# Performance work log

Hardware: AMD Instinct MI355X
Metric: run time of the kernel (lower is better)

The kernel has to match this reference:

```python
import jax, jax.numpy as jnp
import numpy as np

CUTOFF = 3  # cutoff_freq default in low_pass_filter


def _low_pass(x):
    # full 2D FFT over (H, W), keep only the 4 corner blocks of size CUTOFF
    H, W = x.shape[-2], x.shape[-1]
    f = jnp.fft.fftn(x, axes=(-2, -1))
    mask = jnp.zeros((H, W), dtype=x.dtype)
    c = CUTOFF
    mask = mask.at[:c, :c].set(1).at[:c, -c:].set(1).at[-c:, :c].set(1).at[-c:, -c:].set(1)
    return jnp.abs(jnp.fft.ifftn(f * mask, axes=(-2, -1)))


def setup_inputs() -> dict:
    key = jax.random.key(0)
    k_x, k_w1, k_b1, k_w2, k_b2 = jax.random.split(key, 5)
    n_feat = 8
    B, C, H, W = 32, 3, 512, 512
    x = jax.random.uniform(k_x, (B, C, H, W), dtype=jnp.float32)
    # 1x1 convs == channel-mixing matrices; kaiming-ish scale
    w1 = jax.random.normal(k_w1, (n_feat, C), dtype=jnp.float32) * (1.0 / np.sqrt(C))
    b1 = jax.random.normal(k_b1, (n_feat,), dtype=jnp.float32) * 0.01
    w2 = jax.random.normal(k_w2, (C, n_feat), dtype=jnp.float32) * (1.0 / np.sqrt(n_feat))
    b2 = jax.random.normal(k_b2, (C,), dtype=jnp.float32) * 0.01
    return {"x": x, "w1": w1, "b1": b1, "w2": w2, "b2": b2}


def reference(x, w1, b1, w2, b2):
    lp = _low_pass(x)                                        # [B,3,H,W]
    h = jax.nn.relu(jnp.einsum('bchw,fc->bfhw', lp, w1) + b1[None, :, None, None])
    y = jnp.einsum('bfhw,cf->bchw', h, w2) + b2[None, :, None, None]
    return jnp.clip(y + lp, 0.0, 1.0)
```

## Files before the change

### kernel.cpp

```cpp
#include <hip/hip_runtime.h>
#include <math.h>


#define WS_TS 0
#define WS_F  6144
#define WS_A  12288
constexpr int NPART = 8;
constexpr int ROWS = 32;

__global__ __launch_bounds__(256) void k_tab(float* __restrict__ ws) {
    int h = blockIdx.x * 256 + threadIdx.x;
    if (h >= 512) return;
    const float STEP = 6.28318530717958647692f / 512.0f;
    const int mv[6] = {0, 1, 2, -3, -2, -1};
    float* tsp = ws + WS_TS + h * 12;
#pragma unroll
    for (int i = 0; i < 6; ++i) {
        int r = ((mv[i] * h) % 512 + 512) & 511;
        float s, c;
        sincosf(STEP * (float)r, &s, &c);
        tsp[2 * i] = c; tsp[2 * i + 1] = s;
    }
}

__global__ __launch_bounds__(256) void k_colsum(const float* __restrict__ x,
                                                float* __restrict__ ws) {
    __shared__ float Xc[128][29];
    float* A = ws + WS_A;
    int img = blockIdx.x >> 3;
    int hgp = blockIdx.x & 7;
    int t = threadIdx.x;
    int wq = t & 127;
    int hl = t >> 7;
    int h0 = (hgp * 2 + hl) * ROWS;
    const float* xp = x + (size_t)img * 262144 + (size_t)h0 * 512 + wq * 4;

    const float TH = 6.28318530717958647692f / 512.0f;
    float pc1, ps1, pc2, ps2, pc3, ps3;
    sincosf(TH * (float)h0, &ps1, &pc1);
    pc2 = pc1 * pc1 - ps1 * ps1;  ps2 = 2.f * pc1 * ps1;
    pc3 = pc1 * pc2 - ps1 * ps2;  ps3 = ps1 * pc2 + pc1 * ps2;
    const float C1 = 0.99992470183914450299f, S1 = 0.01227153828571992539f;
    const float C2 = 0.99969881869620422012f, S2 = 0.02454122852291228803f;
    const float C3 = 0.99932238458834954375f, S3 = 0.03680722294135883171f;

    float s0[4] = {0,0,0,0};
    float ar1[4] = {0,0,0,0}, ai1[4] = {0,0,0,0};
    float ar2[4] = {0,0,0,0}, ai2[4] = {0,0,0,0};
    float ar3[4] = {0,0,0,0}, ai3[4] = {0,0,0,0};

#pragma unroll 4
    for (int i = 0; i < ROWS; ++i) {
        float4 xv = *(const float4*)(xp + (size_t)i * 512);
        float xa[4] = {xv.x, xv.y, xv.z, xv.w};
#pragma unroll
        for (int q = 0; q < 4; ++q) {
            s0[q] += xa[q];
            ar1[q] = fmaf(xa[q], pc1, ar1[q]);  ai1[q] = fmaf(-xa[q], ps1, ai1[q]);
            ar2[q] = fmaf(xa[q], pc2, ar2[q]);  ai2[q] = fmaf(-xa[q], ps2, ai2[q]);
            ar3[q] = fmaf(xa[q], pc3, ar3[q]);  ai3[q] = fmaf(-xa[q], ps3, ai3[q]);
        }
        float n;
        n = pc1 * C1 - ps1 * S1;  ps1 = ps1 * C1 + pc1 * S1;  pc1 = n;
        n = pc2 * C2 - ps2 * S2;  ps2 = ps2 * C2 + pc2 * S2;  pc2 = n;
        n = pc3 * C3 - ps3 * S3;  ps3 = ps3 * C3 + pc3 * S3;  pc3 = n;
    }

    if (hl == 1) {
        float* r = &Xc[wq][0];
#pragma unroll
        for (int q = 0; q < 4; ++q) {
            r[q]      = s0[q];
            r[4 + q]  = ar1[q];  r[8 + q]  = ai1[q];
            r[12 + q] = ar2[q];  r[16 + q] = ai2[q];
            r[20 + q] = ar3[q];  r[24 + q] = ai3[q];
        }
    }
    __syncthreads();
    if (hl == 0) {
        const float* r = &Xc[wq][0];
        float* Ab = A + (((size_t)img * NPART + hgp) * 8) * 512 + wq * 4;
        *(float4*)(Ab + 0 * 512) = make_float4(s0[0] + r[0], s0[1] + r[1], s0[2] + r[2], s0[3] + r[3]);
        *(float4*)(Ab + 1 * 512) = make_float4(0.f, 0.f, 0.f, 0.f);
        *(float4*)(Ab + 2 * 512) = make_float4(ar1[0] + r[4],  ar1[1] + r[5],  ar1[2] + r[6],  ar1[3] + r[7]);
        *(float4*)(Ab + 3 * 512) = make_float4(ai1[0] + r[8],  ai1[1] + r[9],  ai1[2] + r[10], ai1[3] + r[11]);
        *(float4*)(Ab + 4 * 512) = make_float4(ar2[0] + r[12], ar2[1] + r[13], ar2[2] + r[14], ar2[3] + r[15]);
        *(float4*)(Ab + 5 * 512) = make_float4(ai2[0] + r[16], ai2[1] + r[17], ai2[2] + r[18], ai2[3] + r[19]);
        *(float4*)(Ab + 6 * 512) = make_float4(ar3[0] + r[20], ar3[1] + r[21], ar3[2] + r[22], ar3[3] + r[23]);
        *(float4*)(Ab + 7 * 512) = make_float4(ai3[0] + r[24], ai3[1] + r[25], ai3[2] + r[26], ai3[3] + r[27]);
    }
}

__global__ __launch_bounds__(256) void k_proj(float* __restrict__ ws) {
    __shared__ float As[8][8][68];
    __shared__ float Rs[28][8][2];
    const float* A = ws + WS_A;
    float* F = ws + WS_F;
    int img = blockIdx.x;
    int t = threadIdx.x;

    {
        int plane = t >> 5;
        int w0 = (t & 31) * 16;
        float4 acc[4];
#pragma unroll
        for (int q = 0; q < 4; ++q) acc[q] = make_float4(0.f, 0.f, 0.f, 0.f);
        const float* base = A + ((size_t)img * NPART * 8 + plane) * 512 + w0;
        for (int hg = 0; hg < NPART; ++hg) {
            const float* p = base + (size_t)hg * 8 * 512;
#pragma unroll
            for (int q = 0; q < 4; ++q) {
                float4 v = *(const float4*)(p + q * 4);
                acc[q].x += v.x; acc[q].y += v.y; acc[q].z += v.z; acc[q].w += v.w;
            }
        }
        int seg = w0 >> 6, j0 = w0 & 63;
#pragma unroll
        for (int q = 0; q < 4; ++q)
            *(float4*)&As[plane][seg][j0 + q * 4] = acc[q];
    }
    __syncthreads();

    if (t < 224) {
        int pair = t >> 3, seg = t & 7;
        int k = pair / 7, mi = pair % 7;
        float m = (float)(mi - 3);
        const float TH = 6.28318530717958647692f / 512.0f;
        float cm, sm, pc, ps;
        sincosf(-m * TH, &sm, &cm);
        sincosf(-m * TH * (float)(seg * 64), &ps, &pc);
        const float* Ar_ = &As[2 * k][seg][0];
        const float* Ai_ = &As[2 * k + 1][seg][0];
        float pre = 0.f, pim = 0.f;
#pragma unroll 4
        for (int j = 0; j < 64; ++j) {
            float Ar = Ar_[j], Ai = Ai_[j];
            pre += Ar * pc - Ai * ps;
            pim += Ar * ps + Ai * pc;
            float n = pc * cm - ps * sm;
            ps = ps * cm + pc * sm;
            pc = n;
        }
        Rs[pair][seg][0] = pre;
        Rs[pair][seg][1] = pim;
    }
    __syncthreads();
    if (t < 56) {
        int pair = t >> 1, part = t & 1;
        float s = 0.f;
#pragma unroll
        for (int g = 0; g < 8; ++g) s += Rs[pair][g][part];
        F[(size_t)img * 56 + t] = s;
    }
}

__global__ __launch_bounds__(256) void k_out(const float* __restrict__ ws,
                                             const float* __restrict__ w1,
                                             const float* __restrict__ b1,
                                             const float* __restrict__ w2,
                                             const float* __restrict__ b2,
                                             float* __restrict__ out) {
    const float* tabS = ws + WS_TS;
    const float* Fb = ws + WS_F;
    __shared__ float F_lds[3][56];
    __shared__ float T[4][3][12];
    int t = threadIdx.x;
    int blk = blockIdx.x;
    int b = blk >> 7;
    int h0 = (blk & 127) << 2;

    if (t < 168) {
        int c = t / 56, comp = t % 56;
        F_lds[c][comp] = Fb[(size_t)(b * 3 + c) * 56 + comp];
    }

    float rw1[8][3], rb1[8], rw2[3][8], rb2[3];
#pragma unroll
    for (int f_ = 0; f_ < 8; ++f_) {
        rb1[f_] = b1[f_];
#pragma unroll
        for (int c = 0; c < 3; ++c) rw1[f_][c] = w1[f_ * 3 + c];
    }
#pragma unroll
    for (int c = 0; c < 3; ++c) {
        rb2[c] = b2[c];
#pragma unroll
        for (int f_ = 0; f_ < 8; ++f_) rw2[c][f_] = w2[c * 8 + f_];
    }
    __syncthreads();

    if (t < 72) {
        int rl = t / 18, rem = t % 18;
        int c = rem / 6, kc = rem % 6;
        int h = h0 + rl;
        const float* th = tabS + h * 12;
        int m_kc = (kc < 3) ? kc : kc - 6;
        const float inv = 1.0f / (512.0f * 512.0f);
        float tre = 0.f, tim = 0.f;
#pragma unroll
        for (int kr = 0; kr < 6; ++kr) {
            int kk, mi; float csign;
            if (kr < 3) { kk = kr;     mi = m_kc + 3; csign =  1.f; }
            else        { kk = 6 - kr; mi = 3 - m_kc; csign = -1.f; }
            int pair = kk * 7 + mi;
            float fr = F_lds[c][pair * 2] * inv;
            float fi = F_lds[c][pair * 2 + 1] * csign * inv;
            float cc = th[kr * 2], ss = th[kr * 2 + 1];
            tre += fr * cc - fi * ss;
            tim += fr * ss + fi * cc;
        }
        T[rl][c][kc * 2]     = tre;
        T[rl][c][kc * 2 + 1] = tim;
    }
    __syncthreads();

    int rl = t >> 6, lane = t & 63;
    int h = h0 + rl;
    float A0r[3], A0i[3], U1r[3], U1i[3], V1r[3], V1i[3];
    float U2r[3], U2i[3], V2r[3], V2i[3], Br[3], Bi[3];
#pragma unroll
    for (int c = 0; c < 3; ++c) {
        const float* Tc = T[rl][c];
        A0r[c] = Tc[0];  A0i[c] = Tc[1];
        float t1r = Tc[2],  t1i = Tc[3];
        float t2r = Tc[4],  t2i = Tc[5];
        float bmr = Tc[6],  bmi = Tc[7];
        float m2r = Tc[8],  m2i = Tc[9];
        float m1r = Tc[10], m1i = Tc[11];
        U1r[c] = t1r + m1r; U1i[c] = t1i + m1i;
        V1r[c] = t1r - m1r; V1i[c] = t1i - m1i;
        U2r[c] = t2r + m2r; U2i[c] = t2i + m2i;
        V2r[c] = t2r - m2r; V2i[c] = t2i - m2i;
        Br[c] = bmr; Bi[c] = bmi;
    }
    const float* tw = tabS + lane * 12;
    float c1 = tw[2], s1 = tw[3];
    float c2 = tw[4], s2 = tw[5];
    float c3 = tw[6], s3 = -tw[7];
    const float K = 0.70710678118654752440f;
    float* ob = out + ((size_t)(b * 3) * 512 + h) * 512;

#pragma unroll
    for (int j = 0; j < 8; ++j) {
        int w = lane + 64 * j;
        float lp[3];
#pragma unroll
        for (int c = 0; c < 3; ++c) {
            float re = A0r[c] + U1r[c] * c1 - V1i[c] * s1
                              + U2r[c] * c2 - V2i[c] * s2
                              + Br[c] * c3 + Bi[c] * s3;
            float im = A0i[c] + U1i[c] * c1 + V1r[c] * s1
                              + U2i[c] * c2 + V2r[c] * s2
                              + Bi[c] * c3 - Br[c] * s3;
            lp[c] = sqrtf(re * re + im * im);
        }
        float hid[8];
#pragma unroll
        for (int f_ = 0; f_ < 8; ++f_) {
            float v = rb1[f_] + lp[0] * rw1[f_][0] + lp[1] * rw1[f_][1] + lp[2] * rw1[f_][2];
            hid[f_] = fmaxf(v, 0.0f);
        }
#pragma unroll
        for (int c = 0; c < 3; ++c) {
            float y = rb2[c] + lp[c];
#pragma unroll
            for (int f_ = 0; f_ < 8; ++f_) y += hid[f_] * rw2[c][f_];
            y = fminf(fmaxf(y, 0.0f), 1.0f);
            ob[(size_t)c * 262144 + w] = y;
        }
        if (j < 7) {
            float nc1 = K * (c1 - s1), ns1 = K * (c1 + s1);
            float nc2 = -s2,           ns2 = c2;
            float nc3 = -K * (c3 + s3), ns3 = K * (c3 - s3);
            c1 = nc1; s1 = ns1; c2 = nc2; s2 = ns2; c3 = nc3; s3 = ns3;
        }
    }
}

extern "C" void kernel_launch(void* const* d_in, const int* in_sizes, int n_in,
                              void* d_out, int out_size, void* d_ws, size_t ws_size,
                              hipStream_t stream) {
    const float* x  = (const float*)d_in[0];
    const float* w1 = (const float*)d_in[1];
    const float* b1 = (const float*)d_in[2];
    const float* w2 = (const float*)d_in[3];
    const float* b2 = (const float*)d_in[4];
    float* out = (float*)d_out;
    float* ws = (float*)d_ws;

    hipLaunchKernelGGL(k_tab, dim3(2), dim3(256), 0, stream, ws);
    hipLaunchKernelGGL(k_colsum, dim3(96 * 8), dim3(256), 0, stream, x, ws);
    hipLaunchKernelGGL(k_proj, dim3(96), dim3(256), 0, stream, ws);
    hipLaunchKernelGGL(k_out, dim3(4096), dim3(256), 0, stream, ws, w1, b1, w2, b2, out);
}
```

Baseline: 71.02 us.

## Widen colsum blocks with register prefetch and fold twiddle table into proj

The column-sum kernel now uses 512 threads per block, with four row-groups of 16 rows each instead of two of 32. It prefetches the next four rows into registers while the current four are accumulated, and reduces the partial sums through a larger shared buffer. The twiddle-table kernel is removed and its work moved to an extra block of k_proj, saving one launch. This trades a shorter dependency chain and more memory-level parallelism for extra register pressure and a larger shared reduction.

```diff
diff --git a/kernel.cpp b/kernel.cpp
--- a/kernel.cpp
+++ b/kernel.cpp
@@ -6,33 +6,17 @@
 #define WS_F  6144
 #define WS_A  12288
 constexpr int NPART = 8;
-constexpr int ROWS = 32;
-
-__global__ __launch_bounds__(256) void k_tab(float* __restrict__ ws) {
-    int h = blockIdx.x * 256 + threadIdx.x;
-    if (h >= 512) return;
-    const float STEP = 6.28318530717958647692f / 512.0f;
-    const int mv[6] = {0, 1, 2, -3, -2, -1};
-    float* tsp = ws + WS_TS + h * 12;
-#pragma unroll
-    for (int i = 0; i < 6; ++i) {
-        int r = ((mv[i] * h) % 512 + 512) & 511;
-        float s, c;
-        sincosf(STEP * (float)r, &s, &c);
-        tsp[2 * i] = c; tsp[2 * i + 1] = s;
-    }
-}
-
-__global__ __launch_bounds__(256) void k_colsum(const float* __restrict__ x,
-                                                float* __restrict__ ws) {
-    __shared__ float Xc[128][29];
+
+__global__ __launch_bounds__(512, 6) void k_colsum(const float* __restrict__ x,
+                                                   float* __restrict__ ws) {
+    __shared__ float buf[3][128][29];
     float* A = ws + WS_A;
     int img = blockIdx.x >> 3;
-    int hgp = blockIdx.x & 7;
+    int slab = blockIdx.x & 7;
     int t = threadIdx.x;
     int wq = t & 127;
-    int hl = t >> 7;
-    int h0 = (hgp * 2 + hl) * ROWS;
+    int q = t >> 7;
+    int h0 = slab * 64 + q * 16;
     const float* xp = x + (size_t)img * 262144 + (size_t)h0 * 512 + wq * 4;
 
     const float TH = 6.28318530717958647692f / 512.0f;
@@ -49,75 +33,112 @@
     float ar2[4] = {0,0,0,0}, ai2[4] = {0,0,0,0};
     float ar3[4] = {0,0,0,0}, ai3[4] = {0,0,0,0};
 
-#pragma unroll 4
-    for (int i = 0; i < ROWS; ++i) {
-        float4 xv = *(const float4*)(xp + (size_t)i * 512);
-        float xa[4] = {xv.x, xv.y, xv.z, xv.w};
-#pragma unroll
-        for (int q = 0; q < 4; ++q) {
-            s0[q] += xa[q];
-            ar1[q] = fmaf(xa[q], pc1, ar1[q]);  ai1[q] = fmaf(-xa[q], ps1, ai1[q]);
-            ar2[q] = fmaf(xa[q], pc2, ar2[q]);  ai2[q] = fmaf(-xa[q], ps2, ai2[q]);
-            ar3[q] = fmaf(xa[q], pc3, ar3[q]);  ai3[q] = fmaf(-xa[q], ps3, ai3[q]);
-        }
-        float n;
-        n = pc1 * C1 - ps1 * S1;  ps1 = ps1 * C1 + pc1 * S1;  pc1 = n;
-        n = pc2 * C2 - ps2 * S2;  ps2 = ps2 * C2 + pc2 * S2;  pc2 = n;
-        n = pc3 * C3 - ps3 * S3;  ps3 = ps3 * C3 + pc3 * S3;  pc3 = n;
-    }
-
-    if (hl == 1) {
-        float* r = &Xc[wq][0];
-#pragma unroll
-        for (int q = 0; q < 4; ++q) {
-            r[q]      = s0[q];
-            r[4 + q]  = ar1[q];  r[8 + q]  = ai1[q];
-            r[12 + q] = ar2[q];  r[16 + q] = ai2[q];
-            r[20 + q] = ar3[q];  r[24 + q] = ai3[q];
-        }
-    }
-    __syncthreads();
-    if (hl == 0) {
-        const float* r = &Xc[wq][0];
-        float* Ab = A + (((size_t)img * NPART + hgp) * 8) * 512 + wq * 4;
-        *(float4*)(Ab + 0 * 512) = make_float4(s0[0] + r[0], s0[1] + r[1], s0[2] + r[2], s0[3] + r[3]);
+    float4 cur[4], nxt[4];
+#pragma unroll
+    for (int j = 0; j < 4; ++j) cur[j] = *(const float4*)(xp + (size_t)j * 512);
+#pragma unroll
+    for (int g = 0; g < 4; ++g) {
+        if (g < 3) {
+#pragma unroll
+            for (int j = 0; j < 4; ++j)
+                nxt[j] = *(const float4*)(xp + (size_t)((g + 1) * 4 + j) * 512);
+        }
+#pragma unroll
+        for (int j = 0; j < 4; ++j) {
+            float xa[4] = {cur[j].x, cur[j].y, cur[j].z, cur[j].w};
+#pragma unroll
+            for (int u = 0; u < 4; ++u) {
+                s0[u] += xa[u];
+                ar1[u] = fmaf(xa[u], pc1, ar1[u]);  ai1[u] = fmaf(-xa[u], ps1, ai1[u]);
+                ar2[u] = fmaf(xa[u], pc2, ar2[u]);  ai2[u] = fmaf(-xa[u], ps2, ai2[u]);
+                ar3[u] = fmaf(xa[u], pc3, ar3[u]);  ai3[u] = fmaf(-xa[u], ps3, ai3[u]);
+            }
+            float n;
+            n = pc1 * C1 - ps1 * S1;  ps1 = ps1 * C1 + pc1 * S1;  pc1 = n;
+            n = pc2 * C2 - ps2 * S2;  ps2 = ps2 * C2 + pc2 * S2;  pc2 = n;
+            n = pc3 * C3 - ps3 * S3;  ps3 = ps3 * C3 + pc3 * S3;  pc3 = n;
+        }
+#pragma unroll
+        for (int j = 0; j < 4; ++j) cur[j] = nxt[j];
+    }
+
+    if (q != 0) {
+        float* r = &buf[q - 1][wq][0];
+#pragma unroll
+        for (int u = 0; u < 4; ++u) {
+            r[u]      = s0[u];
+            r[4 + u]  = ar1[u];  r[8 + u]  = ai1[u];
+            r[12 + u] = ar2[u];  r[16 + u] = ai2[u];
+            r[20 + u] = ar3[u];  r[24 + u] = ai3[u];
+        }
+    }
+    __syncthreads();
+    if (q == 0) {
+#pragma unroll
+        for (int v = 0; v < 3; ++v) {
+            const float* r = &buf[v][wq][0];
+#pragma unroll
+            for (int u = 0; u < 4; ++u) {
+                s0[u]  += r[u];
+                ar1[u] += r[4 + u];   ai1[u] += r[8 + u];
+                ar2[u] += r[12 + u];  ai2[u] += r[16 + u];
+                ar3[u] += r[20 + u];  ai3[u] += r[24 + u];
+            }
+        }
+        float* Ab = A + (((size_t)img * NPART + slab) * 8) * 512 + wq * 4;
+        *(float4*)(Ab + 0 * 512) = make_float4(s0[0], s0[1], s0[2], s0[3]);
         *(float4*)(Ab + 1 * 512) = make_float4(0.f, 0.f, 0.f, 0.f);
-        *(float4*)(Ab + 2 * 512) = make_float4(ar1[0] + r[4],  ar1[1] + r[5],  ar1[2] + r[6],  ar1[3] + r[7]);
-        *(float4*)(Ab + 3 * 512) = make_float4(ai1[0] + r[8],  ai1[1] + r[9],  ai1[2] + r[10], ai1[3] + r[11]);
-        *(float4*)(Ab + 4 * 512) = make_float4(ar2[0] + r[12], ar2[1] + r[13], ar2[2] + r[14], ar2[3] + r[15]);
-        *(float4*)(Ab + 5 * 512) = make_float4(ai2[0] + r[16], ai2[1] + r[17], ai2[2] + r[18], ai2[3] + r[19]);
-        *(float4*)(Ab + 6 * 512) = make_float4(ar3[0] + r[20], ar3[1] + r[21], ar3[2] + r[22], ar3[3] + r[23]);
-        *(float4*)(Ab + 7 * 512) = make_float4(ai3[0] + r[24], ai3[1] + r[25], ai3[2] + r[26], ai3[3] + r[27]);
+        *(float4*)(Ab + 2 * 512) = make_float4(ar1[0], ar1[1], ar1[2], ar1[3]);
+        *(float4*)(Ab + 3 * 512) = make_float4(ai1[0], ai1[1], ai1[2], ai1[3]);
+        *(float4*)(Ab + 4 * 512) = make_float4(ar2[0], ar2[1], ar2[2], ar2[3]);
+        *(float4*)(Ab + 5 * 512) = make_float4(ai2[0], ai2[1], ai2[2], ai2[3]);
+        *(float4*)(Ab + 6 * 512) = make_float4(ar3[0], ar3[1], ar3[2], ar3[3]);
+        *(float4*)(Ab + 7 * 512) = make_float4(ai3[0], ai3[1], ai3[2], ai3[3]);
     }
 }
 
 __global__ __launch_bounds__(256) void k_proj(float* __restrict__ ws) {
+    int t = threadIdx.x;
+    if (blockIdx.x == 96) {
+        const float STEP = 6.28318530717958647692f / 512.0f;
+        const int mv[6] = {0, 1, 2, -3, -2, -1};
+        for (int h = t; h < 512; h += 256) {
+            float* tsp = ws + WS_TS + h * 12;
+#pragma unroll
+            for (int i = 0; i < 6; ++i) {
+                int r = ((mv[i] * h) % 512 + 512) & 511;
+                float s, c;
+                sincosf(STEP * (float)r, &s, &c);
+                tsp[2 * i] = c; tsp[2 * i + 1] = s;
+            }
+        }
+        return;
+    }
     __shared__ float As[8][8][68];
     __shared__ float Rs[28][8][2];
     const float* A = ws + WS_A;
     float* F = ws + WS_F;
     int img = blockIdx.x;
-    int t = threadIdx.x;
 
     {
         int plane = t >> 5;
         int w0 = (t & 31) * 16;
         float4 acc[4];
 #pragma unroll
-        for (int q = 0; q < 4; ++q) acc[q] = make_float4(0.f, 0.f, 0.f, 0.f);
+        for (int u = 0; u < 4; ++u) acc[u] = make_float4(0.f, 0.f, 0.f, 0.f);
         const float* base = A + ((size_t)img * NPART * 8 + plane) * 512 + w0;
         for (int hg = 0; hg < NPART; ++hg) {
             const float* p = base + (size_t)hg * 8 * 512;
 #pragma unroll
-            for (int q = 0; q < 4; ++q) {
-                float4 v = *(const float4*)(p + q * 4);
-                acc[q].x += v.x; acc[q].y += v.y; acc[q].z += v.z; acc[q].w += v.w;
+            for (int u = 0; u < 4; ++u) {
+                float4 v = *(const float4*)(p + u * 4);
+                acc[u].x += v.x; acc[u].y += v.y; acc[u].z += v.z; acc[u].w += v.w;
             }
         }
         int seg = w0 >> 6, j0 = w0 & 63;
 #pragma unroll
-        for (int q = 0; q < 4; ++q)
-            *(float4*)&As[plane][seg][j0 + q * 4] = acc[q];
+        for (int u = 0; u < 4; ++u)
+            *(float4*)&As[plane][seg][j0 + u * 4] = acc[u];
     }
     __syncthreads();
 
@@ -288,8 +309,7 @@
     float* out = (float*)d_out;
     float* ws = (float*)d_ws;
 
-    hipLaunchKernelGGL(k_tab, dim3(2), dim3(256), 0, stream, ws);
-    hipLaunchKernelGGL(k_colsum, dim3(96 * 8), dim3(256), 0, stream, x, ws);
-    hipLaunchKernelGGL(k_proj, dim3(96), dim3(256), 0, stream, ws);
+    hipLaunchKernelGGL(k_colsum, dim3(96 * NPART), dim3(512), 0, stream, x, ws);
+    hipLaunchKernelGGL(k_proj, dim3(97), dim3(256), 0, stream, ws);
     hipLaunchKernelGGL(k_out, dim3(4096), dim3(256), 0, stream, ws, w1, b1, w2, b2, out);
 }
```

Result: no change. 69.74 us (-1.8%).

## Restructure column-sum loads, split projection across segments, fold table into proj

Applied to the files above, without the earlier changes.

k_colsum now uses 4 waves per block, each handling 16 rows with two float4 loads per row (two column halves), batched loads of 8 rows, and twiddles recomputed per row from a base angle. Partials from the other waves are reduced through shared memory. k_proj is split into 8 blocks per image, one per 64-column segment, and the final segment sum moves into k_out. The twiddle table kernel is folded into an extra block of k_proj, which removes one launch. These changes aim to raise memory-level parallelism and increase block count on the small stages, at the cost of extra partial-sum traffic and more registers.

```diff
diff --git a/kernel.cpp b/kernel.cpp
--- a/kernel.cpp
+++ b/kernel.cpp
@@ -3,134 +3,162 @@
 
 
 #define WS_TS 0
-#define WS_F  6144
-#define WS_A  12288
+#define WS_PP 8192
+#define WS_A  65536
 constexpr int NPART = 8;
-constexpr int ROWS = 32;
-
-__global__ __launch_bounds__(256) void k_tab(float* __restrict__ ws) {
-    int h = blockIdx.x * 256 + threadIdx.x;
-    if (h >= 512) return;
-    const float STEP = 6.28318530717958647692f / 512.0f;
-    const int mv[6] = {0, 1, 2, -3, -2, -1};
-    float* tsp = ws + WS_TS + h * 12;
-#pragma unroll
-    for (int i = 0; i < 6; ++i) {
-        int r = ((mv[i] * h) % 512 + 512) & 511;
-        float s, c;
-        sincosf(STEP * (float)r, &s, &c);
-        tsp[2 * i] = c; tsp[2 * i + 1] = s;
-    }
-}
-
-__global__ __launch_bounds__(256) void k_colsum(const float* __restrict__ x,
-                                                float* __restrict__ ws) {
-    __shared__ float Xc[128][29];
+
+#define CJ1 0.99992470183914450299f
+#define CJ2 0.99969881869620422012f
+#define CJ3 0.99932238458834954375f
+#define CJ4 0.99879545620517239271f
+#define SJ1 0.01227153828571992539f
+#define SJ2 0.02454122852291228803f
+#define SJ3 0.03680722294135883171f
+#define SJ4 0.04906767432741801425f
+
+__global__ __launch_bounds__(256, 4) void k_colsum(const float* __restrict__ x,
+                                                   float* __restrict__ ws) {
+    __shared__ float buf[3][64][57];
     float* A = ws + WS_A;
     int img = blockIdx.x >> 3;
-    int hgp = blockIdx.x & 7;
+    int hgrp = blockIdx.x & 7;
     int t = threadIdx.x;
-    int wq = t & 127;
-    int hl = t >> 7;
-    int h0 = (hgp * 2 + hl) * ROWS;
-    const float* xp = x + (size_t)img * 262144 + (size_t)h0 * 512 + wq * 4;
+    int v = t >> 6;
+    int lane = t & 63;
+    int R0 = hgrp * 64 + v * 16;
+    const float* xb = x + (size_t)img * 262144 + (size_t)R0 * 512 + lane * 4;
 
     const float TH = 6.28318530717958647692f / 512.0f;
-    float pc1, ps1, pc2, ps2, pc3, ps3;
-    sincosf(TH * (float)h0, &ps1, &pc1);
-    pc2 = pc1 * pc1 - ps1 * ps1;  ps2 = 2.f * pc1 * ps1;
-    pc3 = pc1 * pc2 - ps1 * ps2;  ps3 = ps1 * pc2 + pc1 * ps2;
-    const float C1 = 0.99992470183914450299f, S1 = 0.01227153828571992539f;
-    const float C2 = 0.99969881869620422012f, S2 = 0.02454122852291228803f;
-    const float C3 = 0.99932238458834954375f, S3 = 0.03680722294135883171f;
-
-    float s0[4] = {0,0,0,0};
-    float ar1[4] = {0,0,0,0}, ai1[4] = {0,0,0,0};
-    float ar2[4] = {0,0,0,0}, ai2[4] = {0,0,0,0};
-    float ar3[4] = {0,0,0,0}, ai3[4] = {0,0,0,0};
-
-#pragma unroll 4
-    for (int i = 0; i < ROWS; ++i) {
-        float4 xv = *(const float4*)(xp + (size_t)i * 512);
-        float xa[4] = {xv.x, xv.y, xv.z, xv.w};
-#pragma unroll
-        for (int q = 0; q < 4; ++q) {
-            s0[q] += xa[q];
-            ar1[q] = fmaf(xa[q], pc1, ar1[q]);  ai1[q] = fmaf(-xa[q], ps1, ai1[q]);
-            ar2[q] = fmaf(xa[q], pc2, ar2[q]);  ai2[q] = fmaf(-xa[q], ps2, ai2[q]);
-            ar3[q] = fmaf(xa[q], pc3, ar3[q]);  ai3[q] = fmaf(-xa[q], ps3, ai3[q]);
-        }
-        float n;
-        n = pc1 * C1 - ps1 * S1;  ps1 = ps1 * C1 + pc1 * S1;  pc1 = n;
-        n = pc2 * C2 - ps2 * S2;  ps2 = ps2 * C2 + pc2 * S2;  pc2 = n;
-        n = pc3 * C3 - ps3 * S3;  ps3 = ps3 * C3 + pc3 * S3;  pc3 = n;
-    }
-
-    if (hl == 1) {
-        float* r = &Xc[wq][0];
-#pragma unroll
-        for (int q = 0; q < 4; ++q) {
-            r[q]      = s0[q];
-            r[4 + q]  = ar1[q];  r[8 + q]  = ai1[q];
-            r[12 + q] = ar2[q];  r[16 + q] = ai2[q];
-            r[20 + q] = ar3[q];  r[24 + q] = ai3[q];
-        }
+    float bc, bs;
+    sincosf(TH * (float)R0, &bs, &bc);
+
+    float aA[7][4], aB[7][4];
+#pragma unroll
+    for (int c = 0; c < 7; ++c)
+#pragma unroll
+        for (int q = 0; q < 4; ++q) { aA[c][q] = 0.f; aB[c][q] = 0.f; }
+
+    const float CJr[4] = {1.f, CJ1, CJ2, CJ3};
+    const float SJr[4] = {0.f, SJ1, SJ2, SJ3};
+
+#pragma unroll
+    for (int b = 0; b < 4; ++b) {
+        float4 L[8];
+#pragma unroll
+        for (int rr = 0; rr < 4; ++rr) {
+            L[rr * 2 + 0] = *(const float4*)(xb + (size_t)(b * 4 + rr) * 512);
+            L[rr * 2 + 1] = *(const float4*)(xb + (size_t)(b * 4 + rr) * 512 + 256);
+        }
+#pragma unroll
+        for (int rr = 0; rr < 4; ++rr) {
+            float c1 = bc * CJr[rr] - bs * SJr[rr];
+            float s1 = bs * CJr[rr] + bc * SJr[rr];
+            float c2 = c1 * c1 - s1 * s1;
+            float s2 = 2.f * c1 * s1;
+            float c3 = c1 * c2 - s1 * s2;
+            float s3 = s1 * c2 + c1 * s2;
+            float xa[4] = {L[rr * 2].x, L[rr * 2].y, L[rr * 2].z, L[rr * 2].w};
+            float xbv[4] = {L[rr * 2 + 1].x, L[rr * 2 + 1].y, L[rr * 2 + 1].z, L[rr * 2 + 1].w};
+#pragma unroll
+            for (int q = 0; q < 4; ++q) {
+                aA[0][q] += xa[q];
+                aA[1][q] = fmaf(xa[q], c1, aA[1][q]);  aA[2][q] = fmaf(-xa[q], s1, aA[2][q]);
+                aA[3][q] = fmaf(xa[q], c2, aA[3][q]);  aA[4][q] = fmaf(-xa[q], s2, aA[4][q]);
+                aA[5][q] = fmaf(xa[q], c3, aA[5][q]);  aA[6][q] = fmaf(-xa[q], s3, aA[6][q]);
+                aB[0][q] += xbv[q];
+                aB[1][q] = fmaf(xbv[q], c1, aB[1][q]); aB[2][q] = fmaf(-xbv[q], s1, aB[2][q]);
+                aB[3][q] = fmaf(xbv[q], c2, aB[3][q]); aB[4][q] = fmaf(-xbv[q], s2, aB[4][q]);
+                aB[5][q] = fmaf(xbv[q], c3, aB[5][q]); aB[6][q] = fmaf(-xbv[q], s3, aB[6][q]);
+            }
+        }
+        if (b < 3) {
+            float nb = bc * CJ4 - bs * SJ4;
+            bs = bs * CJ4 + bc * SJ4;
+            bc = nb;
+        }
+    }
+
+    if (v != 0) {
+        float* r = &buf[v - 1][lane][0];
+#pragma unroll
+        for (int c = 0; c < 7; ++c)
+#pragma unroll
+            for (int q = 0; q < 4; ++q) {
+                r[c * 4 + q] = aA[c][q];
+                r[28 + c * 4 + q] = aB[c][q];
+            }
     }
     __syncthreads();
-    if (hl == 0) {
-        const float* r = &Xc[wq][0];
-        float* Ab = A + (((size_t)img * NPART + hgp) * 8) * 512 + wq * 4;
-        *(float4*)(Ab + 0 * 512) = make_float4(s0[0] + r[0], s0[1] + r[1], s0[2] + r[2], s0[3] + r[3]);
-        *(float4*)(Ab + 1 * 512) = make_float4(0.f, 0.f, 0.f, 0.f);
-        *(float4*)(Ab + 2 * 512) = make_float4(ar1[0] + r[4],  ar1[1] + r[5],  ar1[2] + r[6],  ar1[3] + r[7]);
-        *(float4*)(Ab + 3 * 512) = make_float4(ai1[0] + r[8],  ai1[1] + r[9],  ai1[2] + r[10], ai1[3] + r[11]);
-        *(float4*)(Ab + 4 * 512) = make_float4(ar2[0] + r[12], ar2[1] + r[13], ar2[2] + r[14], ar2[3] + r[15]);
-        *(float4*)(Ab + 5 * 512) = make_float4(ai2[0] + r[16], ai2[1] + r[17], ai2[2] + r[18], ai2[3] + r[19]);
-        *(float4*)(Ab + 6 * 512) = make_float4(ar3[0] + r[20], ar3[1] + r[21], ar3[2] + r[22], ar3[3] + r[23]);
-        *(float4*)(Ab + 7 * 512) = make_float4(ai3[0] + r[24], ai3[1] + r[25], ai3[2] + r[26], ai3[3] + r[27]);
+    if (v == 0) {
+#pragma unroll
+        for (int u = 0; u < 3; ++u) {
+            const float* r = &buf[u][lane][0];
+#pragma unroll
+            for (int c = 0; c < 7; ++c)
+#pragma unroll
+                for (int q = 0; q < 4; ++q) {
+                    aA[c][q] += r[c * 4 + q];
+                    aB[c][q] += r[28 + c * 4 + q];
+                }
+        }
+        float* Ab = A + (((size_t)img * NPART + hgrp) * 8) * 512 + lane * 4;
+        const int pl[7] = {0, 2, 3, 4, 5, 6, 7};
+#pragma unroll
+        for (int c = 0; c < 7; ++c) {
+            *(float4*)(Ab + (size_t)pl[c] * 512)       = make_float4(aA[c][0], aA[c][1], aA[c][2], aA[c][3]);
+            *(float4*)(Ab + (size_t)pl[c] * 512 + 256) = make_float4(aB[c][0], aB[c][1], aB[c][2], aB[c][3]);
+        }
+        *(float4*)(Ab + 1 * 512)       = make_float4(0.f, 0.f, 0.f, 0.f);
+        *(float4*)(Ab + 1 * 512 + 256) = make_float4(0.f, 0.f, 0.f, 0.f);
     }
 }
 
 __global__ __launch_bounds__(256) void k_proj(float* __restrict__ ws) {
-    __shared__ float As[8][8][68];
-    __shared__ float Rs[28][8][2];
+    int t = threadIdx.x;
+    const float TH = 6.28318530717958647692f / 512.0f;
+    if (blockIdx.x == 768) {
+        const int mv[6] = {0, 1, 2, -3, -2, -1};
+        for (int h = t; h < 512; h += 256) {
+            float* tsp = ws + WS_TS + h * 12;
+#pragma unroll
+            for (int i = 0; i < 6; ++i) {
+                int r = ((mv[i] * h) % 512 + 512) & 511;
+                float s, c;
+                sincosf(TH * (float)r, &s, &c);
+                tsp[2 * i] = c; tsp[2 * i + 1] = s;
+            }
+        }
+        return;
+    }
+    __shared__ float As[8][64];
     const float* A = ws + WS_A;
-    float* F = ws + WS_F;
-    int img = blockIdx.x;
-    int t = threadIdx.x;
+    float* Pp = ws + WS_PP;
+    int img = blockIdx.x >> 3;
+    int seg = blockIdx.x & 7;
 
     {
         int plane = t >> 5;
-        int w0 = (t & 31) * 16;
-        float4 acc[4];
-#pragma unroll
-        for (int q = 0; q < 4; ++q) acc[q] = make_float4(0.f, 0.f, 0.f, 0.f);
-        const float* base = A + ((size_t)img * NPART * 8 + plane) * 512 + w0;
-        for (int hg = 0; hg < NPART; ++hg) {
-            const float* p = base + (size_t)hg * 8 * 512;
-#pragma unroll
-            for (int q = 0; q < 4; ++q) {
-                float4 v = *(const float4*)(p + q * 4);
-                acc[q].x += v.x; acc[q].y += v.y; acc[q].z += v.z; acc[q].w += v.w;
-            }
-        }
-        int seg = w0 >> 6, j0 = w0 & 63;
-#pragma unroll
-        for (int q = 0; q < 4; ++q)
-            *(float4*)&As[plane][seg][j0 + q * 4] = acc[q];
+        int wl = (t & 31) * 2;
+        float2 L[8];
+#pragma unroll
+        for (int hg = 0; hg < NPART; ++hg)
+            L[hg] = *(const float2*)(A + (((size_t)img * NPART + hg) * 8 + plane) * 512 + seg * 64 + wl);
+        float ax = 0.f, ay = 0.f;
+#pragma unroll
+        for (int hg = 0; hg < NPART; ++hg) { ax += L[hg].x; ay += L[hg].y; }
+        As[plane][wl] = ax;
+        As[plane][wl + 1] = ay;
     }
     __syncthreads();
 
-    if (t < 224) {
-        int pair = t >> 3, seg = t & 7;
-        int k = pair / 7, mi = pair % 7;
+    if (t < 28) {
+        int k = t / 7, mi = t % 7;
         float m = (float)(mi - 3);
-        const float TH = 6.28318530717958647692f / 512.0f;
         float cm, sm, pc, ps;
         sincosf(-m * TH, &sm, &cm);
         sincosf(-m * TH * (float)(seg * 64), &ps, &pc);
-        const float* Ar_ = &As[2 * k][seg][0];
-        const float* Ai_ = &As[2 * k + 1][seg][0];
+        const float* Ar_ = &As[2 * k][0];
+        const float* Ai_ = &As[2 * k + 1][0];
         float pre = 0.f, pim = 0.f;
 #pragma unroll 4
         for (int j = 0; j < 64; ++j) {
@@ -141,16 +169,9 @@
             ps = ps * cm + pc * sm;
             pc = n;
         }
-        Rs[pair][seg][0] = pre;
-        Rs[pair][seg][1] = pim;
-    }
-    __syncthreads();
-    if (t < 56) {
-        int pair = t >> 1, part = t & 1;
-        float s = 0.f;
-#pragma unroll
-        for (int g = 0; g < 8; ++g) s += Rs[pair][g][part];
-        F[(size_t)img * 56 + t] = s;
+        float* o = Pp + ((size_t)img * 8 + seg) * 56;
+        o[t * 2] = pre;
+        o[t * 2 + 1] = pim;
     }
 }
 
@@ -161,7 +182,7 @@
                                              const float* __restrict__ b2,
                                              float* __restrict__ out) {
     const float* tabS = ws + WS_TS;
-    const float* Fb = ws + WS_F;
+    const float* Pp = ws + WS_PP;
     __shared__ float F_lds[3][56];
     __shared__ float T[4][3][12];
     int t = threadIdx.x;
@@ -171,7 +192,11 @@
 
     if (t < 168) {
         int c = t / 56, comp = t % 56;
-        F_lds[c][comp] = Fb[(size_t)(b * 3 + c) * 56 + comp];
+        const float* pp = Pp + ((size_t)(b * 3 + c) * 8) * 56 + comp;
+        float s = 0.f;
+#pragma unroll
+        for (int g = 0; g < 8; ++g) s += pp[g * 56];
+        F_lds[c][comp] = s;
     }
 
     float rw1[8][3], rb1[8], rw2[3][8], rb2[3];
@@ -288,8 +313,7 @@
     float* out = (float*)d_out;
     float* ws = (float*)d_ws;
 
-    hipLaunchKernelGGL(k_tab, dim3(2), dim3(256), 0, stream, ws);
     hipLaunchKernelGGL(k_colsum, dim3(96 * 8), dim3(256), 0, stream, x, ws);
-    hipLaunchKernelGGL(k_proj, dim3(96), dim3(256), 0, stream, ws);
+    hipLaunchKernelGGL(k_proj, dim3(769), dim3(256), 0, stream, ws);
     hipLaunchKernelGGL(k_out, dim3(4096), dim3(256), 0, stream, ws, w1, b1, w2, b2, out);
 }
```

New measurement: 64.54 us. 1.1x faster.
